# Performance work log

Hardware: AMD Instinct MI355X
Metric: run time of the kernel (lower is better)

Reference implementation:

```python
import jax, jax.numpy as jnp
import numpy as np


def _conv(x, w, pad):
    # NCHW conv, stride 1, symmetric padding, no bias (matches AdaPT_Conv2d math)
    return jax.lax.conv_general_dilated(
        x, w, window_strides=(1, 1), padding=[(pad, pad), (pad, pad)],
        dimension_numbers=("NCHW", "OIHW", "NCHW"))


def _maxpool(x, k, s, pad):
    return jax.lax.reduce_window(
        x, -jnp.inf, jax.lax.max,
        window_dimensions=(1, 1, k, k), window_strides=(1, 1, s, s),
        padding=[(0, 0), (0, 0), (pad, pad), (pad, pad)])


def setup_inputs() -> dict:
    key = jax.random.key(0)
    ks = jax.random.split(key, 7)
    B = 16384
    inputs = jax.random.normal(ks[0], (B, 1, 28, 28), dtype=jnp.float32)
    # Kaiming-ish scaled weights, OIHW layout (torch convention)
    def w(k, shape):
        fan_in = shape[1] * shape[2] * shape[3] if len(shape) == 4 else shape[1]
        return jax.random.normal(k, shape, dtype=jnp.float32) * (2.0 / fan_in) ** 0.5
    w1 = w(ks[1], (3, 1, 7, 7))
    w2 = w(ks[2], (8, 3, 5, 5))
    w3 = w(ks[3], (10, 8, 3, 3))
    w4 = w(ks[4], (16, 10, 3, 3))
    w5 = w(ks[5], (24, 16, 3, 3))
    wd = jax.random.normal(ks[6], (10, 9 * 24), dtype=jnp.float32) * (2.0 / 216.0) ** 0.5
    return {"inputs": inputs, "w1": w1, "w2": w2, "w3": w3, "w4": w4, "w5": w5, "wd": wd}


def reference(inputs, w1, w2, w3, w4, w5, wd):
    out = jax.nn.relu(_conv(inputs, w1, 3))            # [B, 3, 28, 28]
    out = jax.nn.relu(_conv(out, w2, 2))               # [B, 8, 28, 28]
    out = _maxpool(out, 3, 2, 1)                       # [B, 8, 14, 14]
    out = jax.nn.relu(_conv(out, w3, 1))               # [B, 10, 14, 14]
    out = jax.nn.relu(_conv(out, w4, 1))               # [B, 16, 14, 14]
    out = _maxpool(out, 3, 2, 1)                       # [B, 16, 7, 7]
    out = jax.nn.relu(_conv(out, w5, 1))               # [B, 24, 7, 7]
    out = _maxpool(out, 3, 2, 0)                       # [B, 24, 3, 3]
    out = out.reshape(out.shape[0], -1)                # [B, 216] (torch Flatten order)
    return out @ wd.T                                  # [B, 10]
```

## Files before the change

### kernel.cpp

```cpp
#include <hip/hip_runtime.h>
#include <hip/hip_bf16.h>

typedef _Float16 half2v __attribute__((ext_vector_type(2)));
typedef _Float16 f16x8 __attribute__((ext_vector_type(8)));
typedef float f32x4 __attribute__((ext_vector_type(4)));
typedef unsigned int u32;

__device__ __forceinline__ float dot2(u32 a, u32 b, float c) {
  float d;
  asm("v_dot2_f32_f16 %0, %1, %2, %3" : "=v"(d) : "v"(a), "v"(b), "v"(c));
  return d;
}
__device__ __forceinline__ u32 pkrtz(float a, float b) {
  return __builtin_bit_cast(u32, __builtin_amdgcn_cvt_pkrtz(a, b));
}
__device__ __forceinline__ u32 pack_relu(float a, float b) {
  u32 p = pkrtz(a, b);
  u32 r;
  asm("v_pk_max_f16 %0, %1, 0" : "=v"(r) : "v"(p));
  return r;
}
__device__ __forceinline__ u32 max2(u32 a, u32 b) {
  half2v x = __builtin_bit_cast(half2v, a);
  half2v y = __builtin_bit_cast(half2v, b);
  x.x = (y.x > x.x) ? y.x : x.x;
  x.y = (y.y > x.y) ? y.y : x.y;
  return __builtin_bit_cast(u32, x);
}
__device__ __forceinline__ int imin(int a, int b) { return a < b ? a : b; }

#define W1F 0
#define W2F 512
#define W3F 1536
#define W4F 2304
#define W5F 3584
#define WDF 6144
#define WTOT 7224

__global__ void __launch_bounds__(256) prep_weights(
    const float* __restrict__ w1, const float* __restrict__ w2,
    const float* __restrict__ w3, const float* __restrict__ w4,
    const float* __restrict__ w5, const float* __restrict__ wd,
    u32* __restrict__ wp) {
  int i = threadIdx.x + blockIdx.x * 256;
  if (i < 512) {
    int g = i >> 8, rem = i & 255, l = rem >> 2, r = rem & 3;
    int s = l >> 4, co = l & 15;
    float v[2];
    #pragma unroll
    for (int e = 0; e < 2; ++e) {
      int k = g * 32 + 8 * s + 2 * r + e;
      int p = k >> 1;
      int ky = p >> 2, kx = ((p & 3) << 1) + (k & 1);
      v[e] = (co < 3 && ky < 7 && kx < 7) ? w1[co * 49 + ky * 7 + kx] : 0.0f;
    }
    wp[W1F + i] = pkrtz(v[0], v[1]);
  } else if (i < 1536) {
    int q = i - W2F;
    int g = q >> 8, rem = q & 255, l = rem >> 2, r = rem & 3;
    int s = l >> 4, co = l & 15;
    float v[2];
    #pragma unroll
    for (int e = 0; e < 2; ++e) {
      int k = g * 32 + 8 * s + 2 * r + e;
      int t = k >> 2, ci = k & 3;
      v[e] = (co < 8 && ci < 3 && t < 25) ? w2[co * 75 + ci * 25 + t] : 0.0f;
    }
    wp[W2F + q] = pkrtz(v[0], v[1]);
  } else if (i < 2304) {
    int q = i - W3F;
    int g = q >> 8, rem = q & 255, l = rem >> 2, r = rem & 3;
    int s = l >> 4, co = l & 15;
    float v[2];
    #pragma unroll
    for (int e = 0; e < 2; ++e) {
      int k = g * 32 + 8 * s + 2 * r + e;
      int t = k >> 3, ci = k & 7;
      v[e] = (co < 10 && t < 9) ? w3[co * 72 + ci * 9 + t] : 0.0f;
    }
    wp[W3F + q] = pkrtz(v[0], v[1]);
  } else if (i < 3584) {
    int q = i - W4F;
    int g = q >> 8, rem = q & 255, l = rem >> 2, r = rem & 3;
    int s = l >> 4, co = l & 15;
    float v[2];
    #pragma unroll
    for (int e = 0; e < 2; ++e) {
      int k = g * 32 + 8 * s + 2 * r + e;
      int t = k >> 4, ci = k & 15;
      v[e] = (ci < 10 && t < 9) ? w4[co * 90 + ci * 9 + t] : 0.0f;
    }
    wp[W4F + q] = pkrtz(v[0], v[1]);
  } else if (i < 6144) {
    int q = i - W5F;
    int cot = q / 1280, q2 = q % 1280;
    int g = q2 >> 8, rem = q2 & 255, l = rem >> 2, r = rem & 3;
    int s = l >> 4, co = cot * 16 + (l & 15);
    float v[2];
    #pragma unroll
    for (int e = 0; e < 2; ++e) {
      int k = g * 32 + 8 * s + 2 * r + e;
      int t = k >> 4, ci = k & 15;
      v[e] = (co < 24 && t < 9) ? w5[co * 144 + ci * 9 + t] : 0.0f;
    }
    wp[W5F + q] = pkrtz(v[0], v[1]);
  } else if (i < WTOT) {
    int j = i - WDF;
    int o = j / 108, r = j % 108, cp = r / 9, s = r % 9;
    wp[WDF + j] = pkrtz(wd[o * 216 + (2 * cp) * 9 + s],
                        wd[o * 216 + (2 * cp + 1) * 9 + s]);
  }
}

#define AR_A 3600
#define AR_B 2048
#define SMEMN (AR_A + AR_B)

__device__ __forceinline__ f32x4 mfma16(uint4 a, uint4 b, f32x4 c) {
  return __builtin_amdgcn_mfma_f32_16x16x32_f16(
      __builtin_bit_cast(f16x8, a), __builtin_bit_cast(f16x8, b), c, 0, 0, 0);
}

__global__ void __launch_bounds__(256) mnist_fused(
    const float* __restrict__ in, const u32* __restrict__ wp,
    float* __restrict__ out) {
  __shared__ __align__(16) u32 smem[SMEMN];
  const int t = threadIdx.x;
  const int lane = t & 63;
  const int wid = t >> 6;
  const long long b = blockIdx.x;
  u32* SA = smem;
  u32* SB = smem + AR_A;

  const int s_ = lane >> 4, pxg = lane & 15;

  {
    uint4 z = {0, 0, 0, 0};
    uint4* za = (uint4*)SA;
    uint4* zb = (uint4*)SB;
    for (int i = t; i < 350; i += 256) za[i] = z;
    for (int i = t; i < 512; i += 256) zb[i] = z;
  }
  __syncthreads();

  {
    const float* inb = in + b * 784;
    _Float16* H0 = (_Float16*)SA;
    _Float16* H1 = (_Float16*)(SA + 700);
    for (int p = t; p < 784; p += 256) {
      int y = p / 28, x = p % 28;
      _Float16 h = (_Float16)inb[p];
      int sy = y + 3, sx = x + 3;
      H0[sy * 40 + sx] = h;
      H1[sy * 40 + sx - 1] = h;
    }
  }
  __syncthreads();

  {
    uint4 af[2];
    const uint4* wq = (const uint4*)(wp + W1F);
    af[0] = wq[lane];
    af[1] = wq[64 + lane];
    #pragma unroll 1
    for (int j = wid; j < 56; j += 4) {
      int y = j >> 1;
      int x = ((j & 1) << 4) + pxg;
      const u32* base = SA + ((x & 1) ? 700 : 0) + (x >> 1);
      f32x4 acc = {0.f, 0.f, 0.f, 0.f};
      #pragma unroll
      for (int g = 0; g < 2; ++g) {
        const u32* rp = base + (y + 4 * g + s_) * 20;
        uint4 bv = {rp[0], rp[1], rp[2], rp[3]};
        acc = mfma16(af[g], bv, acc);
      }
      if (s_ == 0 && x < 28) {
        int ob = ((y + 2) * 32 + (x + 2)) * 2;
        SB[ob] = pack_relu(acc[0], acc[1]);
        SB[ob + 1] = pack_relu(acc[2], acc[3]);
      }
    }
  }
  __syncthreads();

  {
    uint4 z = {0, 0, 0, 0};
    uint4* za = (uint4*)SA;
    for (int i = t; i < 900; i += 256) za[i] = z;
  }
  __syncthreads();

  {
    uint4 af[4];
    const uint4* wq = (const uint4*)(wp + W2F);
    #pragma unroll
    for (int g = 0; g < 4; ++g) af[g] = wq[g * 64 + lane];
    int ro0[4], ro1[4];
    #pragma unroll
    for (int g = 0; g < 4; ++g) {
      int t0 = imin(g * 8 + 2 * s_, 24), t1 = imin(g * 8 + 2 * s_ + 1, 24);
      ro0[g] = ((t0 / 5) * 32 + t0 % 5) * 2;
      ro1[g] = ((t1 / 5) * 32 + t1 % 5) * 2;
    }
    #pragma unroll 1
    for (int j = wid; j < 56; j += 4) {
      int y = j >> 1;
      int x = ((j & 1) << 4) + pxg;
      int ab = (y * 32 + x) * 2;
      f32x4 acc = {0.f, 0.f, 0.f, 0.f};
      #pragma unroll
      for (int g = 0; g < 4; ++g) {
        uint2 lo = *(const uint2*)(SB + ab + ro0[g]);
        uint2 hi = *(const uint2*)(SB + ab + ro1[g]);
        uint4 bv = {lo.x, lo.y, hi.x, hi.y};
        acc = mfma16(af[g], bv, acc);
      }
      if (s_ < 2 && x < 28) {
        int ob = ((y + 1) * 30 + (x + 1)) * 4;
        SA[ob + 2 * s_] = pack_relu(acc[0], acc[1]);
        SA[ob + 2 * s_ + 1] = pack_relu(acc[2], acc[3]);
      }
    }
  }
  __syncthreads();

  {
    uint4 z = {0, 0, 0, 0};
    uint4* zb = (uint4*)SB;
    for (int i = t; i < 256; i += 256) zb[i] = z;
  }
  __syncthreads();

  for (int q = t; q < 392; q += 256) {
    int cpp = q & 1, pxq = q >> 1;
    int y = pxq / 14, x = pxq % 14;
    const u32* basep = SA + ((2 * y) * 30 + 2 * x) * 4 + cpp * 2;
    u32 m0 = 0, m1 = 0;
    #pragma unroll
    for (int jj = 0; jj < 3; ++jj)
      #pragma unroll
      for (int kk = 0; kk < 3; ++kk) {
        uint2 v = *(const uint2*)(basep + (jj * 30 + kk) * 4);
        m0 = max2(m0, v.x);
        m1 = max2(m1, v.y);
      }
    uint2 r = {m0, m1};
    *(uint2*)(SB + ((y + 1) * 16 + (x + 1)) * 4 + cpp * 2) = r;
  }
  __syncthreads();

  {
    uint4 z = {0, 0, 0, 0};
    uint4* za = (uint4*)SA;
    for (int i = t; i < 512; i += 256) za[i] = z;
  }
  __syncthreads();

  {
    uint4 af[3];
    const uint4* wq = (const uint4*)(wp + W3F);
    #pragma unroll
    for (int g = 0; g < 3; ++g) af[g] = wq[g * 64 + lane];
    int roff[3];
    #pragma unroll
    for (int g = 0; g < 3; ++g) {
      int tt = imin(g * 4 + s_, 8);
      roff[g] = ((tt / 3) * 16 + tt % 3) * 4;
    }
    #pragma unroll 1
    for (int j = wid; j < 14; j += 4) {
      int y = j;
      int x = pxg;
      int ab = (y * 16 + x) * 4;
      f32x4 acc = {0.f, 0.f, 0.f, 0.f};
      #pragma unroll
      for (int g = 0; g < 3; ++g) {
        uint4 bv = *(const uint4*)(SB + ab + roff[g]);
        acc = mfma16(af[g], bv, acc);
      }
      if (x < 14) {
        int ob = ((y + 1) * 16 + (x + 1)) * 8;
        int cp0 = 2 * s_, cp1 = 2 * s_ + 1;
        u32 p0 = pack_relu(acc[0], acc[1]);
        u32 p1v = pack_relu(acc[2], acc[3]);
        if (cp0 < 5) SA[ob + cp0] = p0;
        if (cp1 < 5) SA[ob + cp1] = p1v;
      }
    }
  }
  __syncthreads();

  {
    uint4 z = {0, 0, 0, 0};
    uint4* zb = (uint4*)SB;
    for (int i = t; i < 512; i += 256) zb[i] = z;
  }
  __syncthreads();

  {
    uint4 af[5];
    const uint4* wq = (const uint4*)(wp + W4F);
    #pragma unroll
    for (int g = 0; g < 5; ++g) af[g] = wq[g * 64 + lane];
    int roff[5];
    #pragma unroll
    for (int g = 0; g < 5; ++g) {
      int tt = imin(g * 2 + (s_ >> 1), 8);
      roff[g] = ((tt / 3) * 16 + tt % 3) * 8 + (s_ & 1) * 4;
    }
    #pragma unroll 1
    for (int j = wid; j < 14; j += 4) {
      int y = j;
      int x = pxg;
      int ab = (y * 16 + x) * 8;
      f32x4 acc = {0.f, 0.f, 0.f, 0.f};
      #pragma unroll
      for (int g = 0; g < 5; ++g) {
        uint4 bv = *(const uint4*)(SA + ab + roff[g]);
        acc = mfma16(af[g], bv, acc);
      }
      if (x < 14) {
        int ob = ((y + 1) * 16 + (x + 1)) * 8;
        SB[ob + 2 * s_] = pack_relu(acc[0], acc[1]);
        SB[ob + 2 * s_ + 1] = pack_relu(acc[2], acc[3]);
      }
    }
  }
  __syncthreads();

  {
    uint4 z = {0, 0, 0, 0};
    uint4* za = (uint4*)SA;
    for (int i = t; i < 162; i += 256) za[i] = z;
  }
  __syncthreads();

  if (t < 98) {
    int cpq = t & 1, pxq = t >> 1;
    int y = pxq / 7, x = pxq % 7;
    const u32* basep = SB + ((2 * y) * 16 + 2 * x) * 8 + cpq * 4;
    u32 m0 = 0, m1 = 0, m2 = 0, m3 = 0;
    #pragma unroll
    for (int jj = 0; jj < 3; ++jj)
      #pragma unroll
      for (int kk = 0; kk < 3; ++kk) {
        uint4 v = *(const uint4*)(basep + (jj * 16 + kk) * 8);
        m0 = max2(m0, v.x);
        m1 = max2(m1, v.y);
        m2 = max2(m2, v.z);
        m3 = max2(m3, v.w);
      }
    uint4 r = {m0, m1, m2, m3};
    *(uint4*)(SA + ((y + 1) * 9 + (x + 1)) * 8 + cpq * 4) = r;
  }
  __syncthreads();

  {
    int roff[5];
    #pragma unroll
    for (int g = 0; g < 5; ++g) {
      int tt = imin(g * 2 + (s_ >> 1), 8);
      roff[g] = ((tt / 3) * 9 + tt % 3) * 8 + (s_ & 1) * 4;
    }
    #pragma unroll 1
    for (int j = wid; j < 14; j += 4) {
      int cot = j > 6 ? 1 : 0;
      int y = j - (cot ? 7 : 0);
      int x = pxg;
      uint4 af[5];
      const uint4* wq = (const uint4*)(wp + W5F + cot * 1280);
      #pragma unroll
      for (int g = 0; g < 5; ++g) af[g] = wq[g * 64 + lane];
      int ab = (y * 9 + x) * 8;
      f32x4 acc = {0.f, 0.f, 0.f, 0.f};
      #pragma unroll
      for (int g = 0; g < 5; ++g) {
        uint4 bv = *(const uint4*)(SA + ab + roff[g]);
        acc = mfma16(af[g], bv, acc);
      }
      if (x < 7 && (cot == 0 || s_ < 2)) {
        int ob = (y * 7 + x) * 12 + cot * 8;
        SB[ob + 2 * s_] = pack_relu(acc[0], acc[1]);
        SB[ob + 2 * s_ + 1] = pack_relu(acc[2], acc[3]);
      }
    }
  }
  __syncthreads();

  if (t < 108) {
    int cp = t % 12, pxq = t / 12;
    int y = pxq / 3, x = pxq % 3;
    const u32* basep = SB + ((2 * y) * 7 + 2 * x) * 12 + cp;
    u32 m = 0;
    #pragma unroll
    for (int jj = 0; jj < 3; ++jj)
      #pragma unroll
      for (int kk = 0; kk < 3; ++kk) m = max2(m, basep[(jj * 7 + kk) * 12]);
    SA[cp * 9 + pxq] = m;
  }
  __syncthreads();

  if (t < 120) {
    int o = t / 12, c = t % 12;
    const u32* wrow = wp + WDF + o * 108 + c * 9;
    float acc = 0.f;
    #pragma unroll
    for (int s = 0; s < 9; ++s) acc = dot2(SA[c * 9 + s], wrow[s], acc);
    ((float*)SA)[128 + o * 12 + c] = acc;
  }
  __syncthreads();
  if (t < 10) {
    const float* par = (const float*)SA + 128 + t * 12;
    float s = 0.f;
    #pragma unroll
    for (int c = 0; c < 12; ++c) s += par[c];
    out[b * 10 + t] = s;
  }
}

extern "C" void kernel_launch(void* const* d_in, const int* in_sizes, int n_in,
                              void* d_out, int out_size, void* d_ws, size_t ws_size,
                              hipStream_t stream) {
  const float* in = (const float*)d_in[0];
  const float* w1 = (const float*)d_in[1];
  const float* w2 = (const float*)d_in[2];
  const float* w3 = (const float*)d_in[3];
  const float* w4 = (const float*)d_in[4];
  const float* w5 = (const float*)d_in[5];
  const float* wd = (const float*)d_in[6];
  u32* wp = (u32*)d_ws;
  float* out = (float*)d_out;
  int B = in_sizes[0] / 784;

  prep_weights<<<(WTOT + 255) / 256, 256, 0, stream>>>(w1, w2, w3, w4, w5, wd, wp);
  mnist_fused<<<B, 256, 0, stream>>>(in, wp, out);
}
```

Measured before the change: 194.8 us.

## Process two pixel tiles per MFMA iteration and trim LDS zeroing

Each wave now computes two 16-pixel tiles per loop iteration in conv1-conv4 (two accumulators sharing the same weight fragments), halving loop trip counts and exposing two independent MFMA chains. The full SA zero-fill before conv2 is replaced with a border-only clear, and the first maxpool handles four channel pairs per thread with 128-bit LDS loads. Conv5 loads activations once and loops over the two output-channel tiles. The aim is fewer barriers-bound iterations, better MFMA latency hiding and less LDS traffic, at the cost of more registers and uneven work across waves.

```diff
diff --git a/kernel.cpp b/kernel.cpp
--- a/kernel.cpp
+++ b/kernel.cpp
@@ -163,30 +163,41 @@
     af[0] = wq[lane];
     af[1] = wq[64 + lane];
     #pragma unroll 1
-    for (int j = wid; j < 56; j += 4) {
-      int y = j >> 1;
-      int x = ((j & 1) << 4) + pxg;
+    for (int j = wid; j < 28; j += 4) {
+      int y = j;
+      int x = pxg;
       const u32* base = SA + ((x & 1) ? 700 : 0) + (x >> 1);
-      f32x4 acc = {0.f, 0.f, 0.f, 0.f};
+      f32x4 acc0 = {0.f, 0.f, 0.f, 0.f};
+      f32x4 acc1 = {0.f, 0.f, 0.f, 0.f};
       #pragma unroll
       for (int g = 0; g < 2; ++g) {
         const u32* rp = base + (y + 4 * g + s_) * 20;
-        uint4 bv = {rp[0], rp[1], rp[2], rp[3]};
-        acc = mfma16(af[g], bv, acc);
-      }
-      if (s_ == 0 && x < 28) {
+        uint4 b0 = {rp[0], rp[1], rp[2], rp[3]};
+        uint4 b1 = {rp[8], rp[9], rp[10], rp[11]};
+        acc0 = mfma16(af[g], b0, acc0);
+        acc1 = mfma16(af[g], b1, acc1);
+      }
+      if (s_ == 0) {
         int ob = ((y + 2) * 32 + (x + 2)) * 2;
-        SB[ob] = pack_relu(acc[0], acc[1]);
-        SB[ob + 1] = pack_relu(acc[2], acc[3]);
-      }
-    }
-  }
-  __syncthreads();
-
-  {
-    uint4 z = {0, 0, 0, 0};
-    uint4* za = (uint4*)SA;
-    for (int i = t; i < 900; i += 256) za[i] = z;
+        SB[ob] = pack_relu(acc0[0], acc0[1]);
+        SB[ob + 1] = pack_relu(acc0[2], acc0[3]);
+        if (x + 16 < 28) {
+          SB[ob + 32] = pack_relu(acc1[0], acc1[1]);
+          SB[ob + 33] = pack_relu(acc1[2], acc1[3]);
+        }
+      }
+    }
+  }
+  __syncthreads();
+
+  if (t < 116) {
+    uint4 z = {0, 0, 0, 0};
+    int idx;
+    if (t < 30) idx = t;
+    else if (t < 60) idx = 870 + (t - 30);
+    else if (t < 88) idx = (t - 59) * 30;
+    else idx = (t - 87) * 30 + 29;
+    ((uint4*)SA)[idx] = z;
   }
   __syncthreads();
 
@@ -203,22 +214,31 @@
       ro1[g] = ((t1 / 5) * 32 + t1 % 5) * 2;
     }
     #pragma unroll 1
-    for (int j = wid; j < 56; j += 4) {
-      int y = j >> 1;
-      int x = ((j & 1) << 4) + pxg;
+    for (int j = wid; j < 28; j += 4) {
+      int y = j;
+      int x = pxg;
       int ab = (y * 32 + x) * 2;
-      f32x4 acc = {0.f, 0.f, 0.f, 0.f};
+      f32x4 acc0 = {0.f, 0.f, 0.f, 0.f};
+      f32x4 acc1 = {0.f, 0.f, 0.f, 0.f};
       #pragma unroll
       for (int g = 0; g < 4; ++g) {
-        uint2 lo = *(const uint2*)(SB + ab + ro0[g]);
-        uint2 hi = *(const uint2*)(SB + ab + ro1[g]);
-        uint4 bv = {lo.x, lo.y, hi.x, hi.y};
-        acc = mfma16(af[g], bv, acc);
-      }
-      if (s_ < 2 && x < 28) {
+        uint2 lo0 = *(const uint2*)(SB + ab + ro0[g]);
+        uint2 hi0 = *(const uint2*)(SB + ab + ro1[g]);
+        uint4 b0 = {lo0.x, lo0.y, hi0.x, hi0.y};
+        acc0 = mfma16(af[g], b0, acc0);
+        uint2 lo1 = *(const uint2*)(SB + ab + 32 + ro0[g]);
+        uint2 hi1 = *(const uint2*)(SB + ab + 32 + ro1[g]);
+        uint4 b1 = {lo1.x, lo1.y, hi1.x, hi1.y};
+        acc1 = mfma16(af[g], b1, acc1);
+      }
+      if (s_ < 2) {
         int ob = ((y + 1) * 30 + (x + 1)) * 4;
-        SA[ob + 2 * s_] = pack_relu(acc[0], acc[1]);
-        SA[ob + 2 * s_ + 1] = pack_relu(acc[2], acc[3]);
+        SA[ob + 2 * s_] = pack_relu(acc0[0], acc0[1]);
+        SA[ob + 2 * s_ + 1] = pack_relu(acc0[2], acc0[3]);
+        if (x + 16 < 28) {
+          SA[ob + 64 + 2 * s_] = pack_relu(acc1[0], acc1[1]);
+          SA[ob + 64 + 2 * s_ + 1] = pack_relu(acc1[2], acc1[3]);
+        }
       }
     }
   }
@@ -231,21 +251,22 @@
   }
   __syncthreads();
 
-  for (int q = t; q < 392; q += 256) {
-    int cpp = q & 1, pxq = q >> 1;
-    int y = pxq / 14, x = pxq % 14;
-    const u32* basep = SA + ((2 * y) * 30 + 2 * x) * 4 + cpp * 2;
-    u32 m0 = 0, m1 = 0;
+  if (t < 196) {
+    int y = t / 14, x = t % 14;
+    const u32* basep = SA + ((2 * y) * 30 + 2 * x) * 4;
+    u32 m0 = 0, m1 = 0, m2 = 0, m3 = 0;
     #pragma unroll
     for (int jj = 0; jj < 3; ++jj)
       #pragma unroll
       for (int kk = 0; kk < 3; ++kk) {
-        uint2 v = *(const uint2*)(basep + (jj * 30 + kk) * 4);
+        uint4 v = *(const uint4*)(basep + (jj * 30 + kk) * 4);
         m0 = max2(m0, v.x);
         m1 = max2(m1, v.y);
-      }
-    uint2 r = {m0, m1};
-    *(uint2*)(SB + ((y + 1) * 16 + (x + 1)) * 4 + cpp * 2) = r;
+        m2 = max2(m2, v.z);
+        m3 = max2(m3, v.w);
+      }
+    uint4 r = {m0, m1, m2, m3};
+    *(uint4*)(SB + ((y + 1) * 16 + (x + 1)) * 4) = r;
   }
   __syncthreads();
 
@@ -268,23 +289,34 @@
       roff[g] = ((tt / 3) * 16 + tt % 3) * 4;
     }
     #pragma unroll 1
-    for (int j = wid; j < 14; j += 4) {
-      int y = j;
+    for (int j = wid; j < 7; j += 4) {
+      int y0 = 2 * j;
       int x = pxg;
-      int ab = (y * 16 + x) * 4;
-      f32x4 acc = {0.f, 0.f, 0.f, 0.f};
+      int ab = (y0 * 16 + x) * 4;
+      f32x4 acc0 = {0.f, 0.f, 0.f, 0.f};
+      f32x4 acc1 = {0.f, 0.f, 0.f, 0.f};
       #pragma unroll
       for (int g = 0; g < 3; ++g) {
-        uint4 bv = *(const uint4*)(SB + ab + roff[g]);
-        acc = mfma16(af[g], bv, acc);
+        uint4 b0 = *(const uint4*)(SB + ab + roff[g]);
+        acc0 = mfma16(af[g], b0, acc0);
+        uint4 b1 = *(const uint4*)(SB + ab + 64 + roff[g]);
+        acc1 = mfma16(af[g], b1, acc1);
       }
       if (x < 14) {
-        int ob = ((y + 1) * 16 + (x + 1)) * 8;
         int cp0 = 2 * s_, cp1 = 2 * s_ + 1;
-        u32 p0 = pack_relu(acc[0], acc[1]);
-        u32 p1v = pack_relu(acc[2], acc[3]);
-        if (cp0 < 5) SA[ob + cp0] = p0;
-        if (cp1 < 5) SA[ob + cp1] = p1v;
+        int ob0 = ((y0 + 1) * 16 + (x + 1)) * 8;
+        u32 p00 = pack_relu(acc0[0], acc0[1]);
+        u32 p01 = pack_relu(acc0[2], acc0[3]);
+        u32 p10 = pack_relu(acc1[0], acc1[1]);
+        u32 p11 = pack_relu(acc1[2], acc1[3]);
+        if (cp0 < 5) {
+          SA[ob0 + cp0] = p00;
+          SA[ob0 + 128 + cp0] = p10;
+        }
+        if (cp1 < 5) {
+          SA[ob0 + cp1] = p01;
+          SA[ob0 + 128 + cp1] = p11;
+        }
       }
     }
   }
@@ -309,20 +341,25 @@
       roff[g] = ((tt / 3) * 16 + tt % 3) * 8 + (s_ & 1) * 4;
     }
     #pragma unroll 1
-    for (int j = wid; j < 14; j += 4) {
-      int y = j;
+    for (int j = wid; j < 7; j += 4) {
+      int y0 = 2 * j;
       int x = pxg;
-      int ab = (y * 16 + x) * 8;
-      f32x4 acc = {0.f, 0.f, 0.f, 0.f};
+      int ab = (y0 * 16 + x) * 8;
+      f32x4 acc0 = {0.f, 0.f, 0.f, 0.f};
+      f32x4 acc1 = {0.f, 0.f, 0.f, 0.f};
       #pragma unroll
       for (int g = 0; g < 5; ++g) {
-        uint4 bv = *(const uint4*)(SA + ab + roff[g]);
-        acc = mfma16(af[g], bv, acc);
+        uint4 b0 = *(const uint4*)(SA + ab + roff[g]);
+        acc0 = mfma16(af[g], b0, acc0);
+        uint4 b1 = *(const uint4*)(SA + ab + 128 + roff[g]);
+        acc1 = mfma16(af[g], b1, acc1);
       }
       if (x < 14) {
-        int ob = ((y + 1) * 16 + (x + 1)) * 8;
-        SB[ob + 2 * s_] = pack_relu(acc[0], acc[1]);
-        SB[ob + 2 * s_ + 1] = pack_relu(acc[2], acc[3]);
+        int ob0 = ((y0 + 1) * 16 + (x + 1)) * 8;
+        SB[ob0 + 2 * s_] = pack_relu(acc0[0], acc0[1]);
+        SB[ob0 + 2 * s_ + 1] = pack_relu(acc0[2], acc0[3]);
+        SB[ob0 + 128 + 2 * s_] = pack_relu(acc1[0], acc1[1]);
+        SB[ob0 + 128 + 2 * s_ + 1] = pack_relu(acc1[2], acc1[3]);
       }
     }
   }
@@ -363,25 +400,27 @@
       roff[g] = ((tt / 3) * 9 + tt % 3) * 8 + (s_ & 1) * 4;
     }
     #pragma unroll 1
-    for (int j = wid; j < 14; j += 4) {
-      int cot = j > 6 ? 1 : 0;
-      int y = j - (cot ? 7 : 0);
+    for (int j = wid; j < 7; j += 4) {
+      int y = j;
       int x = pxg;
-      uint4 af[5];
-      const uint4* wq = (const uint4*)(wp + W5F + cot * 1280);
-      #pragma unroll
-      for (int g = 0; g < 5; ++g) af[g] = wq[g * 64 + lane];
       int ab = (y * 9 + x) * 8;
-      f32x4 acc = {0.f, 0.f, 0.f, 0.f};
-      #pragma unroll
-      for (int g = 0; g < 5; ++g) {
-        uint4 bv = *(const uint4*)(SA + ab + roff[g]);
-        acc = mfma16(af[g], bv, acc);
-      }
-      if (x < 7 && (cot == 0 || s_ < 2)) {
-        int ob = (y * 7 + x) * 12 + cot * 8;
-        SB[ob + 2 * s_] = pack_relu(acc[0], acc[1]);
-        SB[ob + 2 * s_ + 1] = pack_relu(acc[2], acc[3]);
+      uint4 bv[5];
+      #pragma unroll
+      for (int g = 0; g < 5; ++g) bv[g] = *(const uint4*)(SA + ab + roff[g]);
+      #pragma unroll 1
+      for (int cot = 0; cot < 2; ++cot) {
+        uint4 af[5];
+        const uint4* wq = (const uint4*)(wp + W5F + cot * 1280);
+        #pragma unroll
+        for (int g = 0; g < 5; ++g) af[g] = wq[g * 64 + lane];
+        f32x4 acc = {0.f, 0.f, 0.f, 0.f};
+        #pragma unroll
+        for (int g = 0; g < 5; ++g) acc = mfma16(af[g], bv[g], acc);
+        if (x < 7 && (cot == 0 || s_ < 2)) {
+          int ob = (y * 7 + x) * 12 + cot * 8;
+          SB[ob + 2 * s_] = pack_relu(acc[0], acc[1]);
+          SB[ob + 2 * s_ + 1] = pack_relu(acc[2], acc[3]);
+        }
       }
     }
   }
```

Measured after the change: 190.4 us. 2.2% less time.
